# Kernel optimization log

Measured on AMD Instinct MI355X. Metric: run time of the kernel, lower is better.

Reference implementation:

```python
import jax, jax.numpy as jnp
import numpy as np

NEG_SLOPE = 0.01  # torch leaky_relu default


def setup_inputs() -> dict:
    key = jax.random.key(0)
    ks = jax.random.split(key, 13)
    B = 65536
    # weights stored as [in, out] (transposed vs torch Linear, same math)
    def lin(k, i, o):
        kw, kb = jax.random.split(k)
        bound = 1.0 / np.sqrt(i)
        W = jax.random.uniform(kw, (i, o), jnp.float32, -bound, bound)
        b = jax.random.uniform(kb, (o,), jnp.float32, -bound, bound)
        return W, b
    Wh1, bh1 = lin(ks[0], 2, 50)
    Wh2, bh2 = lin(ks[1], 50, 20)
    Wh3, bh3 = lin(ks[2], 20, 2)
    Wx1, bx1 = lin(ks[3], 2, 50)
    Wx2, bx2 = lin(ks[4], 50, 20)
    Wx3, bx3 = lin(ks[5], 20, 2)
    w = jax.random.normal(ks[6], (B, 2), jnp.float32)
    return {
        "w": w,
        "Wh1": Wh1, "bh1": bh1, "Wh2": Wh2, "bh2": bh2, "Wh3": Wh3, "bh3": bh3,
        "Wx1": Wx1, "bx1": bx1, "Wx2": Wx2, "bx2": bx2, "Wx3": Wx3, "bx3": bx3,
        "num_points": 512,
    }


def reference(w, Wh1, bh1, Wh2, bh2, Wh3, bh3,
              Wx1, bx1, Wx2, bx2, Wx3, bx3, num_points):
    lrelu = lambda z: jax.nn.leaky_relu(z, NEG_SLOPE)

    def step(h, _):
        h = lrelu(h @ Wh1 + bh1)   # [B, 50]
        h = lrelu(h @ Wh2 + bh2)   # [B, 20]
        h = lrelu(h @ Wh3 + bh3)   # [B, 2]
        x = jax.nn.sigmoid(h @ Wx1 + bx1)
        x = jax.nn.sigmoid(x @ Wx2 + bx2)
        x = jax.nn.sigmoid(x @ Wx3 + bx3)  # [B, 2]
        return h, x

    _, xs = jax.lax.scan(step, w, None, length=num_points)  # xs: [T, B, 2]
    return jnp.transpose(xs, (1, 0, 2))  # [B, T, 2]
```

## Files before the change

### kernel.cpp

```cpp
#include <hip/hip_runtime.h>

#define LOG2E 1.44269504088896340736f

__device__ __forceinline__ float lrelu(float z) { return fmaxf(z, 0.01f * z); }
__device__ __forceinline__ float sigf(float z) {
    float p = __builtin_amdgcn_exp2f(-LOG2E * z);
    return __builtin_amdgcn_rcpf(1.0f + p);
}

#define WQ(i) __int_as_float(__builtin_amdgcn_readlane(__float_as_int(wreg[(i) >> 6]), (i) & 63))

__global__ void __launch_bounds__(256, 1)
pc8_kernel(const float* __restrict__ w,
           const float* __restrict__ Wh1, const float* __restrict__ bh1,
           const float* __restrict__ Wh2, const float* __restrict__ bh2,
           const float* __restrict__ Wh3, const float* __restrict__ bh3,
           const float* __restrict__ Wx1, const float* __restrict__ bx1,
           const float* __restrict__ Wx2, const float* __restrict__ bx2,
           const float* __restrict__ Wx3, const float* __restrict__ bx3,
           float2* __restrict__ out, int B, int T)
{
    __shared__ float4 sW2h[185];
    __shared__ float4 sW2x[195];
    __shared__ float2 hbuf[2][256];

    {
        float* a = (float*)sW2h;
        for (int i = threadIdx.x; i < 740; i += 256) a[i] = Wh2[i];
        float* b = (float*)sW2x;
        for (int i = threadIdx.x; i < 780; i += 256) b[i] = Wx2[i];
    }

    const int wid  = threadIdx.x >> 6;
    const int lane = threadIdx.x & 63;
    const bool is_f = (wid < 2);

    float wreg[6];
    float wv[140];
    if (is_f) {
#pragma unroll
        for (int r = 0; r < 6; ++r) {
            const int idx = r * 64 + lane;
            float v = 0.f;
            if      (idx < 100) v = Wh1[idx];
            else if (idx < 150) v = bh1[idx - 100];
            else if (idx < 270) v = Wh2[880 + (idx - 150)];
            else if (idx < 290) v = bh2[idx - 270];
            else if (idx < 330) v = Wh3[idx - 290];
            else if (idx < 332) v = bh3[idx - 330];
            wreg[r] = v;
        }
#pragma unroll
        for (int i = 0; i < 140; ++i) {
            wv[i] = Wh2[740 + i];
            asm volatile("" : "+v"(wv[i]));
        }
    } else {
#pragma unroll
        for (int r = 0; r < 6; ++r) {
            const int idx = r * 64 + lane;
            float v = 0.f;
            if      (idx < 100) v = Wx1[idx];
            else if (idx < 150) v = bx1[idx - 100];
            else if (idx < 230) v = Wx2[920 + (idx - 150)];
            else if (idx < 250) v = bx2[idx - 230];
            else if (idx < 290) v = Wx3[idx - 250];
            else if (idx < 292) v = bx3[idx - 290];
            wreg[r] = v;
        }
#pragma unroll
        for (int i = 0; i < 140; ++i) {
            wv[i] = Wx2[780 + i];
            asm volatile("" : "+v"(wv[i]));
        }
    }
    __syncthreads();

    const int lw = is_f ? wid : (wid - 2);
    const int lpA = lw * 128 + lane;
    const int lpB = lpA + 64;
    const int pA  = blockIdx.x * 256 + lpA;
    const int pB  = blockIdx.x * 256 + lpB;

    float hA0 = 0.f, hA1 = 0.f, hB0 = 0.f, hB1 = 0.f;
    if (is_f) {
        hA0 = w[2 * pA]; hA1 = w[2 * pA + 1];
        hB0 = w[2 * pB]; hB1 = w[2 * pB + 1];
    }
    float2* __restrict__ orowA = out + (size_t)pA * (size_t)T;
    float2* __restrict__ orowB = out + (size_t)pB * (size_t)T;

    for (int t = 0; t <= T; ++t) {
        if (is_f) {
            if (t < T) {
                float a1A[50], a1B[50];
#pragma unroll
                for (int j = 0; j < 50; ++j) {
                    const float s0 = WQ(j), s1 = WQ(50 + j), sb = WQ(100 + j);
                    a1A[j] = lrelu(fmaf(hA0, s0, fmaf(hA1, s1, sb)));
                    a1B[j] = lrelu(fmaf(hB0, s0, fmaf(hB1, s1, sb)));
                }
                float accA[20], accB[20];
#pragma unroll
                for (int c = 0; c < 20; ++c) {
                    const float bv = WQ(270 + c);
                    accA[c] = bv; accB[c] = bv;
                }
#pragma unroll
                for (int k = 0; k < 37; ++k) {
                    const float akA = a1A[k], akB = a1B[k];
#pragma unroll
                    for (int c = 0; c < 5; ++c) {
                        const float4 v = sW2h[k * 5 + c];
                        accA[4*c+0] = fmaf(akA, v.x, accA[4*c+0]);
                        accA[4*c+1] = fmaf(akA, v.y, accA[4*c+1]);
                        accA[4*c+2] = fmaf(akA, v.z, accA[4*c+2]);
                        accA[4*c+3] = fmaf(akA, v.w, accA[4*c+3]);
                        accB[4*c+0] = fmaf(akB, v.x, accB[4*c+0]);
                        accB[4*c+1] = fmaf(akB, v.y, accB[4*c+1]);
                        accB[4*c+2] = fmaf(akB, v.z, accB[4*c+2]);
                        accB[4*c+3] = fmaf(akB, v.w, accB[4*c+3]);
                    }
                }
#pragma unroll
                for (int k = 37; k < 44; ++k) {
                    const float akA = a1A[k], akB = a1B[k];
#pragma unroll
                    for (int c = 0; c < 20; ++c) {
                        const float wvv = wv[(k - 37) * 20 + c];
                        accA[c] = fmaf(akA, wvv, accA[c]);
                        accB[c] = fmaf(akB, wvv, accB[c]);
                    }
                }
#pragma unroll
                for (int k = 44; k < 50; ++k) {
                    const float akA = a1A[k], akB = a1B[k];
#pragma unroll
                    for (int c = 0; c < 20; ++c) {
                        const float wvv = WQ(150 + (k - 44) * 20 + c);
                        accA[c] = fmaf(akA, wvv, accA[c]);
                        accB[c] = fmaf(akB, wvv, accB[c]);
                    }
                }
                float zA0 = WQ(330), zA1 = WQ(331);
                float zB0 = zA0, zB1 = zA1;
#pragma unroll
                for (int k = 0; k < 20; ++k) {
                    const float wx = WQ(290 + 2 * k), wy = WQ(291 + 2 * k);
                    const float eA = lrelu(accA[k]), eB = lrelu(accB[k]);
                    zA0 = fmaf(eA, wx, zA0); zA1 = fmaf(eA, wy, zA1);
                    zB0 = fmaf(eB, wx, zB0); zB1 = fmaf(eB, wy, zB1);
                }
                hA0 = lrelu(zA0); hA1 = lrelu(zA1);
                hB0 = lrelu(zB0); hB1 = lrelu(zB1);

                hbuf[t & 1][lpA] = make_float2(hA0, hA1);
                hbuf[t & 1][lpB] = make_float2(hB0, hB1);
            }
        } else {
            if (t > 0) {
                const int s = t - 1;
                const float2 hvA = hbuf[s & 1][lpA];
                const float2 hvB = hbuf[s & 1][lpB];

                float accA[20], accB[20];
#pragma unroll
                for (int c = 0; c < 20; ++c) {
                    const float bv = WQ(230 + c);
                    accA[c] = bv; accB[c] = bv;
                }
#pragma unroll
                for (int k = 0; k < 50; ++k) {
                    const float s0 = WQ(k), s1 = WQ(50 + k), sb = WQ(100 + k);
                    const float xkA = sigf(fmaf(hvA.x, s0, fmaf(hvA.y, s1, sb)));
                    const float xkB = sigf(fmaf(hvB.x, s0, fmaf(hvB.y, s1, sb)));
                    if (k < 39) {
#pragma unroll
                        for (int c = 0; c < 5; ++c) {
                            const float4 v = sW2x[k * 5 + c];
                            accA[4*c+0] = fmaf(xkA, v.x, accA[4*c+0]);
                            accA[4*c+1] = fmaf(xkA, v.y, accA[4*c+1]);
                            accA[4*c+2] = fmaf(xkA, v.z, accA[4*c+2]);
                            accA[4*c+3] = fmaf(xkA, v.w, accA[4*c+3]);
                            accB[4*c+0] = fmaf(xkB, v.x, accB[4*c+0]);
                            accB[4*c+1] = fmaf(xkB, v.y, accB[4*c+1]);
                            accB[4*c+2] = fmaf(xkB, v.z, accB[4*c+2]);
                            accB[4*c+3] = fmaf(xkB, v.w, accB[4*c+3]);
                        }
                    } else if (k < 46) {
#pragma unroll
                        for (int c = 0; c < 20; ++c) {
                            const float wvv = wv[(k - 39) * 20 + c];
                            accA[c] = fmaf(xkA, wvv, accA[c]);
                            accB[c] = fmaf(xkB, wvv, accB[c]);
                        }
                    } else {
#pragma unroll
                        for (int c = 0; c < 20; ++c) {
                            const float wvv = WQ(150 + (k - 46) * 20 + c);
                            accA[c] = fmaf(xkA, wvv, accA[c]);
                            accB[c] = fmaf(xkB, wvv, accB[c]);
                        }
                    }
                }
                float zA0 = WQ(290), zA1 = WQ(291);
                float zB0 = zA0, zB1 = zA1;
#pragma unroll
                for (int k = 0; k < 20; ++k) {
                    const float wx = WQ(250 + 2 * k), wy = WQ(251 + 2 * k);
                    const float eA = sigf(accA[k]), eB = sigf(accB[k]);
                    zA0 = fmaf(eA, wx, zA0); zA1 = fmaf(eA, wy, zA1);
                    zB0 = fmaf(eB, wx, zB0); zB1 = fmaf(eB, wy, zB1);
                }
                orowA[s] = make_float2(sigf(zA0), sigf(zA1));
                orowB[s] = make_float2(sigf(zB0), sigf(zB1));
            }
        }
        __syncthreads();
    }
}

extern "C" void kernel_launch(void* const* d_in, const int* in_sizes, int n_in,
                              void* d_out, int out_size, void* d_ws, size_t ws_size,
                              hipStream_t stream)
{
    const float* w   = (const float*)d_in[0];
    const float* Wh1 = (const float*)d_in[1];
    const float* bh1 = (const float*)d_in[2];
    const float* Wh2 = (const float*)d_in[3];
    const float* bh2 = (const float*)d_in[4];
    const float* Wh3 = (const float*)d_in[5];
    const float* bh3 = (const float*)d_in[6];
    const float* Wx1 = (const float*)d_in[7];
    const float* bx1 = (const float*)d_in[8];
    const float* Wx2 = (const float*)d_in[9];
    const float* bx2 = (const float*)d_in[10];
    const float* Wx3 = (const float*)d_in[11];
    const float* bx3 = (const float*)d_in[12];

    const int B = in_sizes[0] / 2;
    const int T = out_size / (B * 2);

    pc8_kernel<<<B / 256, 256, 0, stream>>>(
        w, Wh1, bh1, Wh2, bh2, Wh3, bh3,
        Wx1, bx1, Wx2, bx2, Wx3, bx3,
        (float2*)d_out, B, T);
}
```

Before: 3.532 ms.

## Batch two timesteps per x-wave pass, split its layer work across iterations

After: 4.060 ms. 14.9% more time.

```diff
diff --git a/kernel.cpp b/kernel.cpp
--- a/kernel.cpp
+++ b/kernel.cpp
@@ -11,18 +11,18 @@
 #define WQ(i) __int_as_float(__builtin_amdgcn_readlane(__float_as_int(wreg[(i) >> 6]), (i) & 63))
 
 __global__ void __launch_bounds__(256, 1)
-pc8_kernel(const float* __restrict__ w,
-           const float* __restrict__ Wh1, const float* __restrict__ bh1,
-           const float* __restrict__ Wh2, const float* __restrict__ bh2,
-           const float* __restrict__ Wh3, const float* __restrict__ bh3,
-           const float* __restrict__ Wx1, const float* __restrict__ bx1,
-           const float* __restrict__ Wx2, const float* __restrict__ bx2,
-           const float* __restrict__ Wx3, const float* __restrict__ bx3,
-           float2* __restrict__ out, int B, int T)
+pc10_kernel(const float* __restrict__ w,
+            const float* __restrict__ Wh1, const float* __restrict__ bh1,
+            const float* __restrict__ Wh2, const float* __restrict__ bh2,
+            const float* __restrict__ Wh3, const float* __restrict__ bh3,
+            const float* __restrict__ Wx1, const float* __restrict__ bx1,
+            const float* __restrict__ Wx2, const float* __restrict__ bx2,
+            const float* __restrict__ Wx3, const float* __restrict__ bx3,
+            float2* __restrict__ out, int B, int T)
 {
     __shared__ float4 sW2h[185];
     __shared__ float4 sW2x[195];
-    __shared__ float2 hbuf[2][256];
+    __shared__ float2 hbuf[4][256];
 
     {
         float* a = (float*)sW2h;
@@ -68,11 +68,6 @@
             else if (idx < 292) v = bx3[idx - 290];
             wreg[r] = v;
         }
-#pragma unroll
-        for (int i = 0; i < 140; ++i) {
-            wv[i] = Wx2[780 + i];
-            asm volatile("" : "+v"(wv[i]));
-        }
     }
     __syncthreads();
 
@@ -90,7 +85,11 @@
     float2* __restrict__ orowA = out + (size_t)pA * (size_t)T;
     float2* __restrict__ orowB = out + (size_t)pB * (size_t)T;
 
-    for (int t = 0; t <= T; ++t) {
+    float2 xh[2][2];
+    float  xacc[2][2][20];
+    const float* __restrict__ gWx2 = Wx2 + 780;
+
+    for (int t = 0; t <= T + 1; ++t) {
         if (is_f) {
             if (t < T) {
                 float a1A[50], a1B[50];
@@ -154,66 +153,112 @@
                 hA0 = lrelu(zA0); hA1 = lrelu(zA1);
                 hB0 = lrelu(zB0); hB1 = lrelu(zB1);
 
-                hbuf[t & 1][lpA] = make_float2(hA0, hA1);
-                hbuf[t & 1][lpB] = make_float2(hB0, hB1);
+                hbuf[t & 3][lpA] = make_float2(hA0, hA1);
+                hbuf[t & 3][lpB] = make_float2(hB0, hB1);
             }
         } else {
-            if (t > 0) {
-                const int s = t - 1;
-                const float2 hvA = hbuf[s & 1][lpA];
-                const float2 hvB = hbuf[s & 1][lpB];
-
-                float accA[20], accB[20];
+            const int s = t - 1;
+            if (s >= 1 && (s & 1) == 1) {
+                xh[0][0] = hbuf[(s - 1) & 3][lpA];
+                xh[0][1] = hbuf[s & 3][lpA];
+                xh[1][0] = hbuf[(s - 1) & 3][lpB];
+                xh[1][1] = hbuf[s & 3][lpB];
 #pragma unroll
                 for (int c = 0; c < 20; ++c) {
                     const float bv = WQ(230 + c);
-                    accA[c] = bv; accB[c] = bv;
-                }
-#pragma unroll
-                for (int k = 0; k < 50; ++k) {
+                    xacc[0][0][c] = bv; xacc[0][1][c] = bv;
+                    xacc[1][0][c] = bv; xacc[1][1][c] = bv;
+                }
+#pragma unroll
+                for (int k = 0; k < 25; ++k) {
                     const float s0 = WQ(k), s1 = WQ(50 + k), sb = WQ(100 + k);
-                    const float xkA = sigf(fmaf(hvA.x, s0, fmaf(hvA.y, s1, sb)));
-                    const float xkB = sigf(fmaf(hvB.x, s0, fmaf(hvB.y, s1, sb)));
+                    float xk[2][2];
+#pragma unroll
+                    for (int p = 0; p < 2; ++p)
+#pragma unroll
+                        for (int q = 0; q < 2; ++q)
+                            xk[p][q] = sigf(fmaf(xh[p][q].x, s0, fmaf(xh[p][q].y, s1, sb)));
+#pragma unroll
+                    for (int c4 = 0; c4 < 5; ++c4) {
+                        const float4 v = sW2x[k * 5 + c4];
+#pragma unroll
+                        for (int p = 0; p < 2; ++p)
+#pragma unroll
+                            for (int q = 0; q < 2; ++q) {
+                                xacc[p][q][4*c4+0] = fmaf(xk[p][q], v.x, xacc[p][q][4*c4+0]);
+                                xacc[p][q][4*c4+1] = fmaf(xk[p][q], v.y, xacc[p][q][4*c4+1]);
+                                xacc[p][q][4*c4+2] = fmaf(xk[p][q], v.z, xacc[p][q][4*c4+2]);
+                                xacc[p][q][4*c4+3] = fmaf(xk[p][q], v.w, xacc[p][q][4*c4+3]);
+                            }
+                    }
+                }
+            } else if (s >= 2 && (s & 1) == 0) {
+#pragma unroll
+                for (int k = 25; k < 50; ++k) {
+                    const float s0 = WQ(k), s1 = WQ(50 + k), sb = WQ(100 + k);
+                    float xk[2][2];
+#pragma unroll
+                    for (int p = 0; p < 2; ++p)
+#pragma unroll
+                        for (int q = 0; q < 2; ++q)
+                            xk[p][q] = sigf(fmaf(xh[p][q].x, s0, fmaf(xh[p][q].y, s1, sb)));
                     if (k < 39) {
 #pragma unroll
-                        for (int c = 0; c < 5; ++c) {
-                            const float4 v = sW2x[k * 5 + c];
-                            accA[4*c+0] = fmaf(xkA, v.x, accA[4*c+0]);
-                            accA[4*c+1] = fmaf(xkA, v.y, accA[4*c+1]);
-                            accA[4*c+2] = fmaf(xkA, v.z, accA[4*c+2]);
-                            accA[4*c+3] = fmaf(xkA, v.w, accA[4*c+3]);
-                            accB[4*c+0] = fmaf(xkB, v.x, accB[4*c+0]);
-                            accB[4*c+1] = fmaf(xkB, v.y, accB[4*c+1]);
-                            accB[4*c+2] = fmaf(xkB, v.z, accB[4*c+2]);
-                            accB[4*c+3] = fmaf(xkB, v.w, accB[4*c+3]);
+                        for (int c4 = 0; c4 < 5; ++c4) {
+                            const float4 v = sW2x[k * 5 + c4];
+#pragma unroll
+                            for (int p = 0; p < 2; ++p)
+#pragma unroll
+                                for (int q = 0; q < 2; ++q) {
+                                    xacc[p][q][4*c4+0] = fmaf(xk[p][q], v.x, xacc[p][q][4*c4+0]);
+                                    xacc[p][q][4*c4+1] = fmaf(xk[p][q], v.y, xacc[p][q][4*c4+1]);
+                                    xacc[p][q][4*c4+2] = fmaf(xk[p][q], v.z, xacc[p][q][4*c4+2]);
+                                    xacc[p][q][4*c4+3] = fmaf(xk[p][q], v.w, xacc[p][q][4*c4+3]);
+                                }
                         }
                     } else if (k < 46) {
 #pragma unroll
                         for (int c = 0; c < 20; ++c) {
-                            const float wvv = wv[(k - 39) * 20 + c];
-                            accA[c] = fmaf(xkA, wvv, accA[c]);
-                            accB[c] = fmaf(xkB, wvv, accB[c]);
+                            const float wvv = gWx2[(k - 39) * 20 + c];
+#pragma unroll
+                            for (int p = 0; p < 2; ++p)
+#pragma unroll
+                                for (int q = 0; q < 2; ++q)
+                                    xacc[p][q][c] = fmaf(xk[p][q], wvv, xacc[p][q][c]);
                         }
                     } else {
 #pragma unroll
                         for (int c = 0; c < 20; ++c) {
                             const float wvv = WQ(150 + (k - 46) * 20 + c);
-                            accA[c] = fmaf(xkA, wvv, accA[c]);
-                            accB[c] = fmaf(xkB, wvv, accB[c]);
-                        }
-                    }
-                }
-                float zA0 = WQ(290), zA1 = WQ(291);
-                float zB0 = zA0, zB1 = zA1;
+#pragma unroll
+                            for (int p = 0; p < 2; ++p)
+#pragma unroll
+                                for (int q = 0; q < 2; ++q)
+                                    xacc[p][q][c] = fmaf(xk[p][q], wvv, xacc[p][q][c]);
+                        }
+                    }
+                }
+                float z0[2][2], z1[2][2];
+#pragma unroll
+                for (int p = 0; p < 2; ++p)
+#pragma unroll
+                    for (int q = 0; q < 2; ++q) { z0[p][q] = WQ(290); z1[p][q] = WQ(291); }
 #pragma unroll
                 for (int k = 0; k < 20; ++k) {
                     const float wx = WQ(250 + 2 * k), wy = WQ(251 + 2 * k);
-                    const float eA = sigf(accA[k]), eB = sigf(accB[k]);
-                    zA0 = fmaf(eA, wx, zA0); zA1 = fmaf(eA, wy, zA1);
-                    zB0 = fmaf(eB, wx, zB0); zB1 = fmaf(eB, wy, zB1);
-                }
-                orowA[s] = make_float2(sigf(zA0), sigf(zA1));
-                orowB[s] = make_float2(sigf(zB0), sigf(zB1));
+#pragma unroll
+                    for (int p = 0; p < 2; ++p)
+#pragma unroll
+                        for (int q = 0; q < 2; ++q) {
+                            const float e = sigf(xacc[p][q][k]);
+                            z0[p][q] = fmaf(e, wx, z0[p][q]);
+                            z1[p][q] = fmaf(e, wy, z1[p][q]);
+                        }
+                }
+                orowA[s - 2] = make_float2(sigf(z0[0][0]), sigf(z1[0][0]));
+                orowA[s - 1] = make_float2(sigf(z0[0][1]), sigf(z1[0][1]));
+                orowB[s - 2] = make_float2(sigf(z0[1][0]), sigf(z1[1][0]));
+                orowB[s - 1] = make_float2(sigf(z0[1][1]), sigf(z1[1][1]));
             }
         }
         __syncthreads();
@@ -241,7 +286,7 @@
     const int B = in_sizes[0] / 2;
     const int T = out_size / (B * 2);
 
-    pc8_kernel<<<B / 256, 256, 0, stream>>>(
+    pc10_kernel<<<B / 256, 256, 0, stream>>>(
         w, Wh1, bh1, Wh2, bh2, Wh3, bh3,
         Wx1, bx1, Wx2, bx2, Wx3, bx3,
         (float2*)d_out, B, T);
```

## Batch two timesteps per barrier in producer-consumer recurrence kernel

Applied to the files above, without the earlier changes.

Result: slower. 8.486 ms (+140.2%).

```diff
diff --git a/kernel.cpp b/kernel.cpp
--- a/kernel.cpp
+++ b/kernel.cpp
@@ -11,18 +11,18 @@
 #define WQ(i) __int_as_float(__builtin_amdgcn_readlane(__float_as_int(wreg[(i) >> 6]), (i) & 63))
 
 __global__ void __launch_bounds__(256, 1)
-pc8_kernel(const float* __restrict__ w,
-           const float* __restrict__ Wh1, const float* __restrict__ bh1,
-           const float* __restrict__ Wh2, const float* __restrict__ bh2,
-           const float* __restrict__ Wh3, const float* __restrict__ bh3,
-           const float* __restrict__ Wx1, const float* __restrict__ bx1,
-           const float* __restrict__ Wx2, const float* __restrict__ bx2,
-           const float* __restrict__ Wx3, const float* __restrict__ bx3,
-           float2* __restrict__ out, int B, int T)
+pc12_kernel(const float* __restrict__ w,
+            const float* __restrict__ Wh1, const float* __restrict__ bh1,
+            const float* __restrict__ Wh2, const float* __restrict__ bh2,
+            const float* __restrict__ Wh3, const float* __restrict__ bh3,
+            const float* __restrict__ Wx1, const float* __restrict__ bx1,
+            const float* __restrict__ Wx2, const float* __restrict__ bx2,
+            const float* __restrict__ Wx3, const float* __restrict__ bx3,
+            float2* __restrict__ out, int B, int T)
 {
     __shared__ float4 sW2h[185];
     __shared__ float4 sW2x[195];
-    __shared__ float2 hbuf[2][256];
+    __shared__ float2 hbuf[4][256];
 
     {
         float* a = (float*)sW2h;
@@ -68,11 +68,6 @@
             else if (idx < 292) v = bx3[idx - 290];
             wreg[r] = v;
         }
-#pragma unroll
-        for (int i = 0; i < 140; ++i) {
-            wv[i] = Wx2[780 + i];
-            asm volatile("" : "+v"(wv[i]));
-        }
     }
     __syncthreads();
 
@@ -90,130 +85,159 @@
     float2* __restrict__ orowA = out + (size_t)pA * (size_t)T;
     float2* __restrict__ orowB = out + (size_t)pB * (size_t)T;
 
-    for (int t = 0; t <= T; ++t) {
+    const float* __restrict__ gWx2 = Wx2 + 780;
+
+    const int P = T / 2;
+    for (int p = 0; p <= P; ++p) {
         if (is_f) {
-            if (t < T) {
-                float a1A[50], a1B[50];
-#pragma unroll
-                for (int j = 0; j < 50; ++j) {
-                    const float s0 = WQ(j), s1 = WQ(50 + j), sb = WQ(100 + j);
-                    a1A[j] = lrelu(fmaf(hA0, s0, fmaf(hA1, s1, sb)));
-                    a1B[j] = lrelu(fmaf(hB0, s0, fmaf(hB1, s1, sb)));
-                }
-                float accA[20], accB[20];
-#pragma unroll
-                for (int c = 0; c < 20; ++c) {
-                    const float bv = WQ(270 + c);
-                    accA[c] = bv; accB[c] = bv;
-                }
-#pragma unroll
-                for (int k = 0; k < 37; ++k) {
-                    const float akA = a1A[k], akB = a1B[k];
-#pragma unroll
-                    for (int c = 0; c < 5; ++c) {
-                        const float4 v = sW2h[k * 5 + c];
-                        accA[4*c+0] = fmaf(akA, v.x, accA[4*c+0]);
-                        accA[4*c+1] = fmaf(akA, v.y, accA[4*c+1]);
-                        accA[4*c+2] = fmaf(akA, v.z, accA[4*c+2]);
-                        accA[4*c+3] = fmaf(akA, v.w, accA[4*c+3]);
-                        accB[4*c+0] = fmaf(akB, v.x, accB[4*c+0]);
-                        accB[4*c+1] = fmaf(akB, v.y, accB[4*c+1]);
-                        accB[4*c+2] = fmaf(akB, v.z, accB[4*c+2]);
-                        accB[4*c+3] = fmaf(akB, v.w, accB[4*c+3]);
-                    }
-                }
-#pragma unroll
-                for (int k = 37; k < 44; ++k) {
-                    const float akA = a1A[k], akB = a1B[k];
+            if (p < P) {
+                for (int half = 0; half < 2; ++half) {
+                    const int t = 2 * p + half;
+                    float a1A[50], a1B[50];
+#pragma unroll
+                    for (int j = 0; j < 50; ++j) {
+                        const float s0 = WQ(j), s1 = WQ(50 + j), sb = WQ(100 + j);
+                        a1A[j] = lrelu(fmaf(hA0, s0, fmaf(hA1, s1, sb)));
+                        a1B[j] = lrelu(fmaf(hB0, s0, fmaf(hB1, s1, sb)));
+                    }
+                    float accA[20], accB[20];
 #pragma unroll
                     for (int c = 0; c < 20; ++c) {
-                        const float wvv = wv[(k - 37) * 20 + c];
-                        accA[c] = fmaf(akA, wvv, accA[c]);
-                        accB[c] = fmaf(akB, wvv, accB[c]);
-                    }
-                }
-#pragma unroll
-                for (int k = 44; k < 50; ++k) {
-                    const float akA = a1A[k], akB = a1B[k];
-#pragma unroll
-                    for (int c = 0; c < 20; ++c) {
-                        const float wvv = WQ(150 + (k - 44) * 20 + c);
-                        accA[c] = fmaf(akA, wvv, accA[c]);
-                        accB[c] = fmaf(akB, wvv, accB[c]);
-                    }
-                }
-                float zA0 = WQ(330), zA1 = WQ(331);
-                float zB0 = zA0, zB1 = zA1;
-#pragma unroll
-                for (int k = 0; k < 20; ++k) {
-                    const float wx = WQ(290 + 2 * k), wy = WQ(291 + 2 * k);
-                    const float eA = lrelu(accA[k]), eB = lrelu(accB[k]);
-                    zA0 = fmaf(eA, wx, zA0); zA1 = fmaf(eA, wy, zA1);
-                    zB0 = fmaf(eB, wx, zB0); zB1 = fmaf(eB, wy, zB1);
-                }
-                hA0 = lrelu(zA0); hA1 = lrelu(zA1);
-                hB0 = lrelu(zB0); hB1 = lrelu(zB1);
-
-                hbuf[t & 1][lpA] = make_float2(hA0, hA1);
-                hbuf[t & 1][lpB] = make_float2(hB0, hB1);
+                        const float bv = WQ(270 + c);
+                        accA[c] = bv; accB[c] = bv;
+                    }
+#pragma unroll
+                    for (int k = 0; k < 37; ++k) {
+                        const float akA = a1A[k], akB = a1B[k];
+#pragma unroll
+                        for (int c = 0; c < 5; ++c) {
+                            const float4 v = sW2h[k * 5 + c];
+                            accA[4*c+0] = fmaf(akA, v.x, accA[4*c+0]);
+                            accA[4*c+1] = fmaf(akA, v.y, accA[4*c+1]);
+                            accA[4*c+2] = fmaf(akA, v.z, accA[4*c+2]);
+                            accA[4*c+3] = fmaf(akA, v.w, accA[4*c+3]);
+                            accB[4*c+0] = fmaf(akB, v.x, accB[4*c+0]);
+                            accB[4*c+1] = fmaf(akB, v.y, accB[4*c+1]);
+                            accB[4*c+2] = fmaf(akB, v.z, accB[4*c+2]);
+                            accB[4*c+3] = fmaf(akB, v.w, accB[4*c+3]);
+                        }
+                    }
+#pragma unroll
+                    for (int k = 37; k < 44; ++k) {
+                        const float akA = a1A[k], akB = a1B[k];
+#pragma unroll
+                        for (int c = 0; c < 20; ++c) {
+                            const float wvv = wv[(k - 37) * 20 + c];
+                            accA[c] = fmaf(akA, wvv, accA[c]);
+                            accB[c] = fmaf(akB, wvv, accB[c]);
+                        }
+                    }
+#pragma unroll
+                    for (int k = 44; k < 50; ++k) {
+                        const float akA = a1A[k], akB = a1B[k];
+#pragma unroll
+                        for (int c = 0; c < 20; ++c) {
+                            const float wvv = WQ(150 + (k - 44) * 20 + c);
+                            accA[c] = fmaf(akA, wvv, accA[c]);
+                            accB[c] = fmaf(akB, wvv, accB[c]);
+                        }
+                    }
+                    float zA0 = WQ(330), zA1 = WQ(331);
+                    float zB0 = zA0, zB1 = zA1;
+#pragma unroll
+                    for (int k = 0; k < 20; ++k) {
+                        const float wx = WQ(290 + 2 * k), wy = WQ(291 + 2 * k);
+                        const float eA = lrelu(accA[k]), eB = lrelu(accB[k]);
+                        zA0 = fmaf(eA, wx, zA0); zA1 = fmaf(eA, wy, zA1);
+                        zB0 = fmaf(eB, wx, zB0); zB1 = fmaf(eB, wy, zB1);
+                    }
+                    hA0 = lrelu(zA0); hA1 = lrelu(zA1);
+                    hB0 = lrelu(zB0); hB1 = lrelu(zB1);
+
+                    hbuf[t & 3][lpA] = make_float2(hA0, hA1);
+                    hbuf[t & 3][lpB] = make_float2(hB0, hB1);
+                }
             }
         } else {
-            if (t > 0) {
-                const int s = t - 1;
-                const float2 hvA = hbuf[s & 1][lpA];
-                const float2 hvB = hbuf[s & 1][lpB];
-
-                float accA[20], accB[20];
+            if (p >= 1) {
+                const int s0i = 2 * p - 2, s1i = 2 * p - 1;
+                const float2 h0A = hbuf[s0i & 3][lpA];
+                const float2 h1A = hbuf[s1i & 3][lpA];
+                const float2 h0B = hbuf[s0i & 3][lpB];
+                const float2 h1B = hbuf[s1i & 3][lpB];
+
+                float acc0A[20], acc0B[20], acc1A[20], acc1B[20];
 #pragma unroll
                 for (int c = 0; c < 20; ++c) {
                     const float bv = WQ(230 + c);
-                    accA[c] = bv; accB[c] = bv;
+                    acc0A[c] = bv; acc0B[c] = bv; acc1A[c] = bv; acc1B[c] = bv;
                 }
 #pragma unroll
                 for (int k = 0; k < 50; ++k) {
                     const float s0 = WQ(k), s1 = WQ(50 + k), sb = WQ(100 + k);
-                    const float xkA = sigf(fmaf(hvA.x, s0, fmaf(hvA.y, s1, sb)));
-                    const float xkB = sigf(fmaf(hvB.x, s0, fmaf(hvB.y, s1, sb)));
+                    const float xk0A = sigf(fmaf(h0A.x, s0, fmaf(h0A.y, s1, sb)));
+                    const float xk0B = sigf(fmaf(h0B.x, s0, fmaf(h0B.y, s1, sb)));
+                    const float xk1A = sigf(fmaf(h1A.x, s0, fmaf(h1A.y, s1, sb)));
+                    const float xk1B = sigf(fmaf(h1B.x, s0, fmaf(h1B.y, s1, sb)));
                     if (k < 39) {
 #pragma unroll
-                        for (int c = 0; c < 5; ++c) {
-                            const float4 v = sW2x[k * 5 + c];
-                            accA[4*c+0] = fmaf(xkA, v.x, accA[4*c+0]);
-                            accA[4*c+1] = fmaf(xkA, v.y, accA[4*c+1]);
-                            accA[4*c+2] = fmaf(xkA, v.z, accA[4*c+2]);
-                            accA[4*c+3] = fmaf(xkA, v.w, accA[4*c+3]);
-                            accB[4*c+0] = fmaf(xkB, v.x, accB[4*c+0]);
-                            accB[4*c+1] = fmaf(xkB, v.y, accB[4*c+1]);
-                            accB[4*c+2] = fmaf(xkB, v.z, accB[4*c+2]);
-                            accB[4*c+3] = fmaf(xkB, v.w, accB[4*c+3]);
+                        for (int c4 = 0; c4 < 5; ++c4) {
+                            const float4 v = sW2x[k * 5 + c4];
+                            acc0A[4*c4+0] = fmaf(xk0A, v.x, acc0A[4*c4+0]);
+                            acc0A[4*c4+1] = fmaf(xk0A, v.y, acc0A[4*c4+1]);
+                            acc0A[4*c4+2] = fmaf(xk0A, v.z, acc0A[4*c4+2]);
+                            acc0A[4*c4+3] = fmaf(xk0A, v.w, acc0A[4*c4+3]);
+                            acc0B[4*c4+0] = fmaf(xk0B, v.x, acc0B[4*c4+0]);
+                            acc0B[4*c4+1] = fmaf(xk0B, v.y, acc0B[4*c4+1]);
+                            acc0B[4*c4+2] = fmaf(xk0B, v.z, acc0B[4*c4+2]);
+                            acc0B[4*c4+3] = fmaf(xk0B, v.w, acc0B[4*c4+3]);
+                            acc1A[4*c4+0] = fmaf(xk1A, v.x, acc1A[4*c4+0]);
+                            acc1A[4*c4+1] = fmaf(xk1A, v.y, acc1A[4*c4+1]);
+                            acc1A[4*c4+2] = fmaf(xk1A, v.z, acc1A[4*c4+2]);
+                            acc1A[4*c4+3] = fmaf(xk1A, v.w, acc1A[4*c4+3]);
+                            acc1B[4*c4+0] = fmaf(xk1B, v.x, acc1B[4*c4+0]);
+                            acc1B[4*c4+1] = fmaf(xk1B, v.y, acc1B[4*c4+1]);
+                            acc1B[4*c4+2] = fmaf(xk1B, v.z, acc1B[4*c4+2]);
+                            acc1B[4*c4+3] = fmaf(xk1B, v.w, acc1B[4*c4+3]);
                         }
                     } else if (k < 46) {
 #pragma unroll
                         for (int c = 0; c < 20; ++c) {
-                            const float wvv = wv[(k - 39) * 20 + c];
-                            accA[c] = fmaf(xkA, wvv, accA[c]);
-                            accB[c] = fmaf(xkB, wvv, accB[c]);
+                            const float wvv = gWx2[(k - 39) * 20 + c];
+                            acc0A[c] = fmaf(xk0A, wvv, acc0A[c]);
+                            acc0B[c] = fmaf(xk0B, wvv, acc0B[c]);
+                            acc1A[c] = fmaf(xk1A, wvv, acc1A[c]);
+                            acc1B[c] = fmaf(xk1B, wvv, acc1B[c]);
                         }
                     } else {
 #pragma unroll
                         for (int c = 0; c < 20; ++c) {
                             const float wvv = WQ(150 + (k - 46) * 20 + c);
-                            accA[c] = fmaf(xkA, wvv, accA[c]);
-                            accB[c] = fmaf(xkB, wvv, accB[c]);
-                        }
-                    }
-                }
-                float zA0 = WQ(290), zA1 = WQ(291);
-                float zB0 = zA0, zB1 = zA1;
+                            acc0A[c] = fmaf(xk0A, wvv, acc0A[c]);
+                            acc0B[c] = fmaf(xk0B, wvv, acc0B[c]);
+                            acc1A[c] = fmaf(xk1A, wvv, acc1A[c]);
+                            acc1B[c] = fmaf(xk1B, wvv, acc1B[c]);
+                        }
+                    }
+                }
+                float z00A = WQ(290), z10A = WQ(291);
+                float z00B = z00A, z10B = z10A;
+                float z01A = z00A, z11A = z10A;
+                float z01B = z00A, z11B = z10A;
 #pragma unroll
                 for (int k = 0; k < 20; ++k) {
                     const float wx = WQ(250 + 2 * k), wy = WQ(251 + 2 * k);
-                    const float eA = sigf(accA[k]), eB = sigf(accB[k]);
-                    zA0 = fmaf(eA, wx, zA0); zA1 = fmaf(eA, wy, zA1);
-                    zB0 = fmaf(eB, wx, zB0); zB1 = fmaf(eB, wy, zB1);
-                }
-                orowA[s] = make_float2(sigf(zA0), sigf(zA1));
-                orowB[s] = make_float2(sigf(zB0), sigf(zB1));
+                    const float e0A = sigf(acc0A[k]), e0B = sigf(acc0B[k]);
+                    const float e1A = sigf(acc1A[k]), e1B = sigf(acc1B[k]);
+                    z00A = fmaf(e0A, wx, z00A); z10A = fmaf(e0A, wy, z10A);
+                    z00B = fmaf(e0B, wx, z00B); z10B = fmaf(e0B, wy, z10B);
+                    z01A = fmaf(e1A, wx, z01A); z11A = fmaf(e1A, wy, z11A);
+                    z01B = fmaf(e1B, wx, z01B); z11B = fmaf(e1B, wy, z11B);
+                }
+                orowA[s0i] = make_float2(sigf(z00A), sigf(z10A));
+                orowB[s0i] = make_float2(sigf(z00B), sigf(z10B));
+                orowA[s1i] = make_float2(sigf(z01A), sigf(z11A));
+                orowB[s1i] = make_float2(sigf(z01B), sigf(z11B));
             }
         }
         __syncthreads();
@@ -241,7 +265,7 @@
     const int B = in_sizes[0] / 2;
     const int T = out_size / (B * 2);
 
-    pc8_kernel<<<B / 256, 256, 0, stream>>>(
+    pc12_kernel<<<B / 256, 256, 0, stream>>>(
         w, Wh1, bh1, Wh2, bh2, Wh3, bh3,
         Wx1, bx1, Wx2, bx2, Wx3, bx3,
         (float2*)d_out, B, T);
```
